# Kernel tuning notes

Measured on AMD Instinct MI355X. Metric: run time of the kernel, lower is better.

## Reference

```python
import jax, jax.numpy as jnp
import numpy as np

HIDDEN = 1024
HEADS = 16
HEAD_DIM = HIDDEN // HEADS
BATCH = 2
SEQ = 2048


def setup_inputs() -> dict:
    key = jax.random.key(0)
    k1, k2, k3 = jax.random.split(key, 3)
    hidden_states = jax.random.normal(k1, (BATCH, SEQ, HIDDEN), dtype=jnp.float32)
    # torch Linear(hidden, 3*hidden) applies x @ W.T; we store the transposed
    # weight directly so the math is x @ W_qkv. Scale ~ fan_in init.
    W_qkv = jax.random.normal(k2, (HIDDEN, 3 * HIDDEN), dtype=jnp.float32) / np.sqrt(HIDDEN)
    W_o = jax.random.normal(k3, (HIDDEN, HIDDEN), dtype=jnp.float32) / np.sqrt(HIDDEN)
    return {"hidden_states": hidden_states, "W_qkv": W_qkv, "W_o": W_o}


def reference(hidden_states, W_qkv, W_o):
    B, S, _ = hidden_states.shape
    scale = 1.0 / np.sqrt(HEAD_DIM)
    qkv = hidden_states @ W_qkv                       # [B, S, 3*H*D]
    qkv = qkv.reshape(B, S, 3, HEADS, HEAD_DIM)
    qkv = jnp.transpose(qkv, (2, 0, 3, 1, 4))         # [3, B, H, S, D]
    q, k, v = qkv[0], qkv[1], qkv[2]
    # The chunked online-softmax path computes exactly softmax(qk^T*scale)v.
    scores = jnp.einsum("bhsd,bhtd->bhst", q, k) * scale  # [B, H, S, S]
    probs = jax.nn.softmax(scores, axis=-1)
    out = jnp.einsum("bhst,bhtd->bhsd", probs, v)     # [B, H, S, D]
    out = jnp.transpose(out, (0, 2, 1, 3)).reshape(B, S, HIDDEN)
    return out @ W_o
```

## Files before the change

### kernel.cpp

```cpp
#include <hip/hip_runtime.h>
#include <hip/hip_bf16.h>
#include <cstdint>

typedef __bf16 bf16_t;
typedef __bf16 bf16x8 __attribute__((ext_vector_type(8)));
typedef __bf16 bf16x4 __attribute__((ext_vector_type(4)));
typedef __bf16 bf16x2 __attribute__((ext_vector_type(2)));
typedef float  f32x4  __attribute__((ext_vector_type(4)));
typedef float  f32x16 __attribute__((ext_vector_type(16)));
typedef unsigned uint4v __attribute__((ext_vector_type(4)));

#define AS1 __attribute__((address_space(1)))
#define AS3 __attribute__((address_space(3)))

static __device__ __forceinline__ void gld_lds16(const void* g, void* l) {
  __builtin_amdgcn_global_load_lds((AS1 void*)g, (AS3 void*)l, 16, 0, 0);
}

static __device__ __forceinline__ unsigned pk2t(float a, float b) {
  return __builtin_amdgcn_perm(__builtin_bit_cast(unsigned, a),
                               __builtin_bit_cast(unsigned, b), 0x03020706u);
}

__global__ __launch_bounds__(256) void prep_k(const float* __restrict__ x,
                                              bf16_t* __restrict__ xb,
                                              const float* __restrict__ wqkv,
                                              bf16_t* __restrict__ wqkvT,
                                              const float* __restrict__ wo,
                                              bf16_t* __restrict__ woT) {
  int bid = blockIdx.x;
  if (bid < 4096) {
    const int i = bid * 256 + threadIdx.x;
    float4 v = ((const float4*)x)[i];
    bf16x4 o;
    o[0] = (bf16_t)v.x; o[1] = (bf16_t)v.y; o[2] = (bf16_t)v.z; o[3] = (bf16_t)v.w;
    *(bf16x4*)(xb + (size_t)i * 4) = o;
    return;
  }
  __shared__ float tile[32][33];
  const float* in; bf16_t* out; int N, bx, by;
  if (bid < 7168) { bid -= 4096; in = wqkv; out = wqkvT; N = 3072; bx = bid % 96; by = bid / 96; }
  else            { bid -= 7168; in = wo;   out = woT;   N = 1024; bx = bid & 31; by = bid >> 5; }
  const int t = threadIdx.x, c = t & 31, r0 = t >> 5;
#pragma unroll
  for (int i = 0; i < 4; ++i) {
    int r = r0 + i * 8;
    tile[r][c] = in[(size_t)(by * 32 + r) * N + bx * 32 + c];
  }
  __syncthreads();
#pragma unroll
  for (int i = 0; i < 4; ++i) {
    int r = r0 + i * 8;
    out[(size_t)(bx * 32 + r) * 1024 + by * 32 + c] = (bf16_t)tile[c][r];
  }
}

template <int KDIM>
static __device__ __forceinline__ void gemm128_pipe(const bf16_t* __restrict__ A,
                                                    const bf16_t* __restrict__ Bt,
                                                    char* lds, f32x4 acc[4][4],
                                                    int bm, int bn) {
  constexpr int NK = KDIM / 32;
  const int t = threadIdx.x;
  const int lr = t & 15, g = (t >> 4) & 3;
  const int w = t >> 6, wr = w >> 1, wc = w & 1;

  auto bufA = [&](int i) { return lds + (i % 3) * 8192; };
  auto bufB = [&](int i) { return lds + 24576 + (i % 3) * 8192; };

  auto stage = [&](int i) {
    const int kt = i * 32;
    char* la = bufA(i);
    char* lb = bufB(i);
#pragma unroll
    for (int c = 0; c < 2; ++c) {
      const int idx = c * 256 + t;
      const int row = idx >> 2, cb = idx & 3;
      const int off = ((t & 192) + c * 256) * 16;
      gld_lds16(A  + (size_t)(bm * 128 + row) * KDIM + kt + cb * 8, la + off);
      gld_lds16(Bt + (size_t)(bn * 128 + row) * KDIM + kt + cb * 8, lb + off);
    }
  };

  stage(0);
  stage(1);
  asm volatile("s_waitcnt vmcnt(4)" ::: "memory");
  __builtin_amdgcn_sched_barrier(0);
  __builtin_amdgcn_s_barrier();

  for (int j = 0; j < NK; ++j) {
    if (j + 2 < NK) {
      stage(j + 2);
      asm volatile("s_waitcnt vmcnt(8)" ::: "memory");
    } else if (j + 1 < NK) {
      asm volatile("s_waitcnt vmcnt(4)" ::: "memory");
    } else {
      asm volatile("s_waitcnt vmcnt(0)" ::: "memory");
    }
    __builtin_amdgcn_sched_barrier(0);
    __builtin_amdgcn_s_barrier();
    const char* laR = bufA(j);
    const char* lbR = bufB(j);
    bf16x8 af[4], bv[4];
#pragma unroll
    for (int mi = 0; mi < 4; ++mi)
      af[mi] = *(const bf16x8*)(laR + (wr * 64 + mi * 16 + lr) * 64 + g * 16);
#pragma unroll
    for (int ni = 0; ni < 4; ++ni)
      bv[ni] = *(const bf16x8*)(lbR + (wc * 64 + ni * 16 + lr) * 64 + g * 16);
    __builtin_amdgcn_s_setprio(1);
#pragma unroll
    for (int mi = 0; mi < 4; ++mi)
#pragma unroll
      for (int ni = 0; ni < 4; ++ni)
        acc[mi][ni] = __builtin_amdgcn_mfma_f32_16x16x32_bf16(af[mi], bv[ni], acc[mi][ni], 0, 0, 0);
    __builtin_amdgcn_s_setprio(0);
    __builtin_amdgcn_sched_barrier(0);
    __builtin_amdgcn_s_barrier();
  }
}

__global__ __launch_bounds__(256) void gemm_qkv_k(const bf16_t* __restrict__ xb,
                                                  const bf16_t* __restrict__ wt,
                                                  bf16_t* __restrict__ Qo,
                                                  bf16_t* __restrict__ Ko,
                                                  bf16_t* __restrict__ Vto) {
  __shared__ __align__(16) char lds[49152];
  const int bm = blockIdx.x, bn = blockIdx.y;
  f32x4 acc[4][4] = {};
  gemm128_pipe<1024>(xb, wt, lds, acc, bm, bn);
  const float cs = 0.18033688011112042f;
  const int t = threadIdx.x, lr = t & 15, g = (t >> 4) & 3, w = t >> 6, wr = w >> 1, wc = w & 1;
  const int row0 = bm * 128 + wr * 64, col0 = bn * 128 + wc * 64;
#pragma unroll
  for (int mi = 0; mi < 4; ++mi) {
    const int row = row0 + mi * 16 + g * 4;
    const int b = row >> 11, s = row & 2047;
#pragma unroll
    for (int ni = 0; ni < 4; ++ni) {
      const int col = col0 + ni * 16 + lr;
      const int t3 = col >> 10, rem = col & 1023, h = rem >> 6, d = rem & 63;
      const int bh = b * 16 + h;
#pragma unroll
      for (int r = 0; r < 4; ++r) {
        const float av = acc[mi][ni][r];
        if (t3 == 0)      Qo[((size_t)bh * 2048 + s + r) * 64 + d] = (bf16_t)(av * cs);
        else if (t3 == 1) Ko[((size_t)bh * 2048 + s + r) * 64 + d] = (bf16_t)av;
        else {
          const int kv = s + r;
          const int q3 = (kv >> 2) & 7;
          const int dq = (q3 & 4) | ((q3 & 1) << 1) | ((q3 >> 1) & 1);
          const int kvp = (kv & ~31) | (dq << 2) | (kv & 3);
          Vto[((size_t)bh * 64 + d) * 2048 + kvp] = (bf16_t)av;
        }
      }
    }
  }
}

__global__ __launch_bounds__(256) void gemm_o_k(const bf16_t* __restrict__ attn,
                                                const bf16_t* __restrict__ wot,
                                                float* __restrict__ out) {
  __shared__ __align__(16) char lds[49152];
  const int bm = blockIdx.x, bn = blockIdx.y;
  f32x4 acc[4][4] = {};
  gemm128_pipe<1024>(attn, wot, lds, acc, bm, bn);
  const int t = threadIdx.x, lr = t & 15, g = (t >> 4) & 3, w = t >> 6, wr = w >> 1, wc = w & 1;
  const int row0 = bm * 128 + wr * 64, col0 = bn * 128 + wc * 64;
#pragma unroll
  for (int mi = 0; mi < 4; ++mi) {
    const int row = row0 + mi * 16 + g * 4;
#pragma unroll
    for (int ni = 0; ni < 4; ++ni) {
      const int col = col0 + ni * 16 + lr;
#pragma unroll
      for (int r = 0; r < 4; ++r)
        out[(size_t)(row + r) * 1024 + col] = acc[mi][ni][r];
    }
  }
}

__global__ __launch_bounds__(256, 2) void attn_k(const bf16_t* __restrict__ Q,
                                                 const bf16_t* __restrict__ K,
                                                 const bf16_t* __restrict__ Vt,
                                                 bf16_t* __restrict__ Ao) {
  __shared__ __align__(16) char smem[32768];
  const int t = threadIdx.x, w = t >> 6, l = t & 63;
  const int ql = l & 31, hi = l >> 5;
  const int orig = blockIdx.y * 16 + blockIdx.x;
  const int swz = (orig & 7) * 64 + (orig >> 3);
  const int qblk = swz & 15, bh = swz >> 4;
  const int b = bh >> 4, h = bh & 15;
  const bf16_t* Qb = Q  + (size_t)bh * 2048 * 64;
  const bf16_t* Kb = K  + (size_t)bh * 2048 * 64;
  const bf16_t* Vb = Vt + (size_t)bh * 64 * 2048;
  const int q0 = qblk * 128 + w * 32;

  const bf16_t* ksrc = Kb + (size_t)l * 64 + w * 8;
  const bf16_t* vsrc = Vb + (size_t)l * 2048 + w * 8;

  char* const kb0 = smem;
  char* const kb1 = smem + 8192;
  char* const vb0 = smem + 16384;
  char* const vb1 = smem + 24576;

  const bf16_t* qp = Qb + (size_t)(q0 + ql) * 64 + hi * 8;
  const bf16x8 qf0 = *(const bf16x8*)(qp);
  const bf16x8 qf1 = *(const bf16x8*)(qp + 16);
  const bf16x8 qf2 = *(const bf16x8*)(qp + 32);
  const bf16x8 qf3 = *(const bf16x8*)(qp + 48);

  bf16x8 ones;
#pragma unroll
  for (int i = 0; i < 8; ++i) ones[i] = (bf16_t)1.0f;

  f32x16 ot0 = {}, ot1 = {}, otls = {};

  auto stageK = [&](int tile, char* dst) {
    const bf16_t* ks = ksrc + (size_t)tile * 4096;
    gld_lds16(ks,      dst + w * 1024);
    gld_lds16(ks + 32, dst + (4 + w) * 1024);
  };
  auto stageV = [&](int tile, char* dst) {
    const bf16_t* vs = vsrc + (size_t)tile * 64;
    gld_lds16(vs,      dst + w * 1024);
    gld_lds16(vs + 32, dst + (4 + w) * 1024);
  };
  auto qk = [&](const char* kbuf, f32x16& sa, f32x16& sb) {
    const bf16x8 ka0 = *(const bf16x8*)(kbuf + (0 + hi) * 1024 + ql * 16);
    const bf16x8 ka1 = *(const bf16x8*)(kbuf + (2 + hi) * 1024 + ql * 16);
    const bf16x8 ka2 = *(const bf16x8*)(kbuf + (4 + hi) * 1024 + ql * 16);
    const bf16x8 ka3 = *(const bf16x8*)(kbuf + (6 + hi) * 1024 + ql * 16);
    sa = __builtin_amdgcn_mfma_f32_32x32x16_bf16(ka0, qf0, sa, 0, 0, 0);
    sa = __builtin_amdgcn_mfma_f32_32x32x16_bf16(ka1, qf1, sa, 0, 0, 0);
    sa = __builtin_amdgcn_mfma_f32_32x32x16_bf16(ka2, qf2, sa, 0, 0, 0);
    sa = __builtin_amdgcn_mfma_f32_32x32x16_bf16(ka3, qf3, sa, 0, 0, 0);
    const bf16x8 kb0f = *(const bf16x8*)(kbuf + (0 + hi) * 1024 + 512 + ql * 16);
    const bf16x8 kb1f = *(const bf16x8*)(kbuf + (2 + hi) * 1024 + 512 + ql * 16);
    const bf16x8 kb2f = *(const bf16x8*)(kbuf + (4 + hi) * 1024 + 512 + ql * 16);
    const bf16x8 kb3f = *(const bf16x8*)(kbuf + (6 + hi) * 1024 + 512 + ql * 16);
    sb = __builtin_amdgcn_mfma_f32_32x32x16_bf16(kb0f, qf0, sb, 0, 0, 0);
    sb = __builtin_amdgcn_mfma_f32_32x32x16_bf16(kb1f, qf1, sb, 0, 0, 0);
    sb = __builtin_amdgcn_mfma_f32_32x32x16_bf16(kb2f, qf2, sb, 0, 0, 0);
    sb = __builtin_amdgcn_mfma_f32_32x32x16_bf16(kb3f, qf3, sb, 0, 0, 0);
  };
  auto sm_pv = [&](const f32x16& sa, const f32x16& sb, const char* vread) {
    uint4v u0 = {pk2t(exp2f(sa[0]),  exp2f(sa[1])),  pk2t(exp2f(sa[2]),  exp2f(sa[3])),
                 pk2t(exp2f(sa[4]),  exp2f(sa[5])),  pk2t(exp2f(sa[6]),  exp2f(sa[7]))};
    uint4v u1 = {pk2t(exp2f(sa[8]),  exp2f(sa[9])),  pk2t(exp2f(sa[10]), exp2f(sa[11])),
                 pk2t(exp2f(sa[12]), exp2f(sa[13])), pk2t(exp2f(sa[14]), exp2f(sa[15]))};
    uint4v u2 = {pk2t(exp2f(sb[0]),  exp2f(sb[1])),  pk2t(exp2f(sb[2]),  exp2f(sb[3])),
                 pk2t(exp2f(sb[4]),  exp2f(sb[5])),  pk2t(exp2f(sb[6]),  exp2f(sb[7]))};
    uint4v u3 = {pk2t(exp2f(sb[8]),  exp2f(sb[9])),  pk2t(exp2f(sb[10]), exp2f(sb[11])),
                 pk2t(exp2f(sb[12]), exp2f(sb[13])), pk2t(exp2f(sb[14]), exp2f(sb[15]))};
    const bf16x8 pf0 = __builtin_bit_cast(bf16x8, u0);
    const bf16x8 pf1 = __builtin_bit_cast(bf16x8, u1);
    const bf16x8 pf2 = __builtin_bit_cast(bf16x8, u2);
    const bf16x8 pf3 = __builtin_bit_cast(bf16x8, u3);
    const bf16x8 v00 = *(const bf16x8*)(vread + (0 + hi) * 1024 + ql * 16);
    const bf16x8 v01 = *(const bf16x8*)(vread + (2 + hi) * 1024 + ql * 16);
    const bf16x8 v02 = *(const bf16x8*)(vread + (4 + hi) * 1024 + ql * 16);
    const bf16x8 v03 = *(const bf16x8*)(vread + (6 + hi) * 1024 + ql * 16);
    const bf16x8 v10 = *(const bf16x8*)(vread + (0 + hi) * 1024 + 512 + ql * 16);
    const bf16x8 v11 = *(const bf16x8*)(vread + (2 + hi) * 1024 + 512 + ql * 16);
    const bf16x8 v12 = *(const bf16x8*)(vread + (4 + hi) * 1024 + 512 + ql * 16);
    const bf16x8 v13 = *(const bf16x8*)(vread + (6 + hi) * 1024 + 512 + ql * 16);
    ot0  = __builtin_amdgcn_mfma_f32_32x32x16_bf16(v00,  pf0, ot0, 0, 0, 0);
    ot1  = __builtin_amdgcn_mfma_f32_32x32x16_bf16(v10,  pf0, ot1, 0, 0, 0);
    otls = __builtin_amdgcn_mfma_f32_32x32x16_bf16(ones, pf0, otls, 0, 0, 0);
    ot0  = __builtin_amdgcn_mfma_f32_32x32x16_bf16(v01,  pf1, ot0, 0, 0, 0);
    ot1  = __builtin_amdgcn_mfma_f32_32x32x16_bf16(v11,  pf1, ot1, 0, 0, 0);
    otls = __builtin_amdgcn_mfma_f32_32x32x16_bf16(ones, pf1, otls, 0, 0, 0);
    ot0  = __builtin_amdgcn_mfma_f32_32x32x16_bf16(v02,  pf2, ot0, 0, 0, 0);
    ot1  = __builtin_amdgcn_mfma_f32_32x32x16_bf16(v12,  pf2, ot1, 0, 0, 0);
    otls = __builtin_amdgcn_mfma_f32_32x32x16_bf16(ones, pf2, otls, 0, 0, 0);
    ot0  = __builtin_amdgcn_mfma_f32_32x32x16_bf16(v03,  pf3, ot0, 0, 0, 0);
    ot1  = __builtin_amdgcn_mfma_f32_32x32x16_bf16(v13,  pf3, ot1, 0, 0, 0);
    otls = __builtin_amdgcn_mfma_f32_32x32x16_bf16(ones, pf3, otls, 0, 0, 0);
  };

  stageK(0, kb0);
  stageV(0, vb0);
  stageK(1, kb1);
  asm volatile("s_waitcnt vmcnt(4)" ::: "memory");
  __builtin_amdgcn_sched_barrier(0);
  __builtin_amdgcn_s_barrier();
  f32x16 sca = {}, scb = {};
  qk(kb0, sca, scb);
  __builtin_amdgcn_s_barrier();

  auto body = [&](int j, char* kstage, const char* kread, const char* vread, char* vstage) {
    if (j < 31) stageV(j + 1, vstage);
    if (j < 30) stageK(j + 2, kstage);
    if (j < 30)      asm volatile("s_waitcnt vmcnt(4)" ::: "memory");
    else if (j == 30) asm volatile("s_waitcnt vmcnt(2)" ::: "memory");
    else             asm volatile("s_waitcnt vmcnt(0)" ::: "memory");
    __builtin_amdgcn_sched_barrier(0);
    __builtin_amdgcn_s_barrier();
    f32x16 sna = {}, snb = {};
    __builtin_amdgcn_s_setprio(1);
    if (j < 31) qk(kread, sna, snb);
    sm_pv(sca, scb, vread);
    __builtin_amdgcn_s_setprio(0);
    __builtin_amdgcn_sched_barrier(0);
    __builtin_amdgcn_s_barrier();
    sca = sna; scb = snb;
  };

#pragma unroll 2
  for (int j = 0; j < 32; ++j) {
    if ((j & 1) == 0) body(j, kb0, kb1, vb0, vb1);
    else              body(j, kb1, kb0, vb1, vb0);
  }

  const float inv = 1.0f / otls[0];
  bf16_t* ob = (bf16_t*)(smem + w * 4096);
#pragma unroll
  for (int rg = 0; rg < 4; ++rg) {
    const int d0 = rg * 8 + hi * 4;
    bf16x4 v0, v1;
#pragma unroll
    for (int j = 0; j < 4; ++j) {
      v0[j] = (bf16_t)(ot0[4 * rg + j] * inv);
      v1[j] = (bf16_t)(ot1[4 * rg + j] * inv);
    }
    *(bf16x4*)((char*)ob + ql * 128 + (((d0)      * 2) ^ ((ql & 7) << 4))) = v0;
    *(bf16x4*)((char*)ob + ql * 128 + (((d0 + 32) * 2) ^ ((ql & 7) << 4))) = v1;
  }
  __syncthreads();
#pragma unroll
  for (int i = 0; i < 4; ++i) {
    const int c = i * 64 + l;
    const int qq = c >> 3, ch = c & 7;
    bf16x8 vv = *(const bf16x8*)((char*)ob + qq * 128 + ((ch * 16) ^ ((qq & 7) << 4)));
    *(bf16x8*)(Ao + (size_t)(b * 2048 + q0 + qq) * 1024 + h * 64 + ch * 8) = vv;
  }
}


extern "C" void kernel_launch(void* const* d_in, const int* in_sizes, int n_in,
                              void* d_out, int out_size, void* d_ws, size_t ws_size,
                              hipStream_t stream) {
  const float* x    = (const float*)d_in[0];
  const float* wqkv = (const float*)d_in[1];
  const float* wo   = (const float*)d_in[2];
  float* out = (float*)d_out;

  char* ws = (char*)d_ws;
  bf16_t* xb    = (bf16_t*)(ws);
  bf16_t* wqkvT = (bf16_t*)(ws + (size_t)(8u  << 20));
  bf16_t* woT   = (bf16_t*)(ws + (size_t)(14u << 20));
  bf16_t* Qb    = (bf16_t*)(ws + (size_t)(16u << 20));
  bf16_t* Kb    = (bf16_t*)(ws + (size_t)(24u << 20));
  bf16_t* Vtb   = (bf16_t*)(ws + (size_t)(32u << 20));
  bf16_t* attn  = (bf16_t*)(ws + (size_t)(40u << 20));

  prep_k<<<8192, 256, 0, stream>>>(x, xb, wqkv, wqkvT, wo, woT);
  gemm_qkv_k<<<dim3(32, 24), 256, 0, stream>>>(xb, wqkvT, Qb, Kb, Vtb);
  attn_k<<<dim3(16, 32), 256, 0, stream>>>(Qb, Kb, Vtb, attn);
  gemm_o_k<<<dim3(32, 8), 256, 0, stream>>>(attn, woT, out);
}
```

Before: 119.0 us.

## Use triple-buffered K/V in attention and a single-barrier GEMM pipeline

The attention kernel moves from double- to triple-buffered K/V tiles in LDS (48KB) and issues the next stages after the per-iteration barrier, which drops the trailing barrier. The GEMM main loop is restructured the same way, with one barrier per k-step and prefetch issued after it. The x fp32-to-bf16 conversion now handles 8 elements per thread, so fewer blocks are launched. The larger LDS footprint per attention block may limit occupancy. Removing the trailing barriers relies on the three-buffer rotation to prevent overwriting tiles that other waves are still reading.

```diff
diff --git a/kernel.cpp b/kernel.cpp
--- a/kernel.cpp
+++ b/kernel.cpp
@@ -29,18 +29,20 @@
                                               const float* __restrict__ wo,
                                               bf16_t* __restrict__ woT) {
   int bid = blockIdx.x;
-  if (bid < 4096) {
+  if (bid < 2048) {
     const int i = bid * 256 + threadIdx.x;
-    float4 v = ((const float4*)x)[i];
-    bf16x4 o;
-    o[0] = (bf16_t)v.x; o[1] = (bf16_t)v.y; o[2] = (bf16_t)v.z; o[3] = (bf16_t)v.w;
-    *(bf16x4*)(xb + (size_t)i * 4) = o;
+    float4 v0 = ((const float4*)x)[(size_t)i * 2];
+    float4 v1 = ((const float4*)x)[(size_t)i * 2 + 1];
+    bf16x8 o;
+    o[0] = (bf16_t)v0.x; o[1] = (bf16_t)v0.y; o[2] = (bf16_t)v0.z; o[3] = (bf16_t)v0.w;
+    o[4] = (bf16_t)v1.x; o[5] = (bf16_t)v1.y; o[6] = (bf16_t)v1.z; o[7] = (bf16_t)v1.w;
+    *(bf16x8*)(xb + (size_t)i * 8) = o;
     return;
   }
   __shared__ float tile[32][33];
   const float* in; bf16_t* out; int N, bx, by;
-  if (bid < 7168) { bid -= 4096; in = wqkv; out = wqkvT; N = 3072; bx = bid % 96; by = bid / 96; }
-  else            { bid -= 7168; in = wo;   out = woT;   N = 1024; bx = bid & 31; by = bid >> 5; }
+  if (bid < 5120) { bid -= 2048; in = wqkv; out = wqkvT; N = 3072; bx = bid % 96; by = bid / 96; }
+  else            { bid -= 5120; in = wo;   out = woT;   N = 1024; bx = bid & 31; by = bid >> 5; }
   const int t = threadIdx.x, c = t & 31, r0 = t >> 5;
 #pragma unroll
   for (int i = 0; i < 4; ++i) {
@@ -84,21 +86,13 @@
 
   stage(0);
   stage(1);
-  asm volatile("s_waitcnt vmcnt(4)" ::: "memory");
-  __builtin_amdgcn_sched_barrier(0);
-  __builtin_amdgcn_s_barrier();
 
   for (int j = 0; j < NK; ++j) {
-    if (j + 2 < NK) {
-      stage(j + 2);
-      asm volatile("s_waitcnt vmcnt(8)" ::: "memory");
-    } else if (j + 1 < NK) {
-      asm volatile("s_waitcnt vmcnt(4)" ::: "memory");
-    } else {
-      asm volatile("s_waitcnt vmcnt(0)" ::: "memory");
-    }
+    if (j < NK - 1) asm volatile("s_waitcnt vmcnt(4)" ::: "memory");
+    else            asm volatile("s_waitcnt vmcnt(0)" ::: "memory");
     __builtin_amdgcn_sched_barrier(0);
     __builtin_amdgcn_s_barrier();
+    if (j + 2 < NK) stage(j + 2);
     const char* laR = bufA(j);
     const char* lbR = bufB(j);
     bf16x8 af[4], bv[4];
@@ -115,8 +109,6 @@
       for (int ni = 0; ni < 4; ++ni)
         acc[mi][ni] = __builtin_amdgcn_mfma_f32_16x16x32_bf16(af[mi], bv[ni], acc[mi][ni], 0, 0, 0);
     __builtin_amdgcn_s_setprio(0);
-    __builtin_amdgcn_sched_barrier(0);
-    __builtin_amdgcn_s_barrier();
   }
 }
 
@@ -184,7 +176,7 @@
                                                  const bf16_t* __restrict__ K,
                                                  const bf16_t* __restrict__ Vt,
                                                  bf16_t* __restrict__ Ao) {
-  __shared__ __align__(16) char smem[32768];
+  __shared__ __align__(16) char smem[49152];
   const int t = threadIdx.x, w = t >> 6, l = t & 63;
   const int ql = l & 31, hi = l >> 5;
   const int orig = blockIdx.y * 16 + blockIdx.x;
@@ -198,11 +190,6 @@
 
   const bf16_t* ksrc = Kb + (size_t)l * 64 + w * 8;
   const bf16_t* vsrc = Vb + (size_t)l * 2048 + w * 8;
-
-  char* const kb0 = smem;
-  char* const kb1 = smem + 8192;
-  char* const vb0 = smem + 16384;
-  char* const vb1 = smem + 24576;
 
   const bf16_t* qp = Qb + (size_t)(q0 + ql) * 64 + hi * 8;
   const bf16x8 qf0 = *(const bf16x8*)(qp);
@@ -279,53 +266,53 @@
     otls = __builtin_amdgcn_mfma_f32_32x32x16_bf16(ones, pf3, otls, 0, 0, 0);
   };
 
-  stageK(0, kb0);
-  stageV(0, vb0);
-  stageK(1, kb1);
-  asm volatile("s_waitcnt vmcnt(4)" ::: "memory");
+  char *k0 = smem,          *k1 = smem + 8192,          *k2 = smem + 16384;
+  char *v0 = smem + 24576,  *v1 = smem + 32768,         *v2 = smem + 40960;
+
+  stageK(0, k0);
+  stageV(0, v0);
+  stageK(1, k1);
+  stageV(1, v1);
+  stageK(2, k2);
+  asm volatile("s_waitcnt vmcnt(8)" ::: "memory");
   __builtin_amdgcn_sched_barrier(0);
   __builtin_amdgcn_s_barrier();
   f32x16 sca = {}, scb = {};
-  qk(kb0, sca, scb);
-  __builtin_amdgcn_s_barrier();
-
-  auto body = [&](int j, char* kstage, const char* kread, const char* vread, char* vstage) {
-    if (j < 31) stageV(j + 1, vstage);
-    if (j < 30) stageK(j + 2, kstage);
-    if (j < 30)      asm volatile("s_waitcnt vmcnt(4)" ::: "memory");
+  qk(k0, sca, scb);
+
+  for (int j = 0; j < 32; ++j) {
+    if (j <= 29)      asm volatile("s_waitcnt vmcnt(4)" ::: "memory");
     else if (j == 30) asm volatile("s_waitcnt vmcnt(2)" ::: "memory");
-    else             asm volatile("s_waitcnt vmcnt(0)" ::: "memory");
+    else              asm volatile("s_waitcnt vmcnt(0)" ::: "memory");
     __builtin_amdgcn_sched_barrier(0);
     __builtin_amdgcn_s_barrier();
+    if (j + 2 < 32) stageV(j + 2, v2);
+    if (j + 3 < 32) stageK(j + 3, k0);
     f32x16 sna = {}, snb = {};
     __builtin_amdgcn_s_setprio(1);
-    if (j < 31) qk(kread, sna, snb);
-    sm_pv(sca, scb, vread);
+    if (j < 31) qk(k1, sna, snb);
+    sm_pv(sca, scb, v0);
     __builtin_amdgcn_s_setprio(0);
-    __builtin_amdgcn_sched_barrier(0);
-    __builtin_amdgcn_s_barrier();
     sca = sna; scb = snb;
-  };
-
-#pragma unroll 2
-  for (int j = 0; j < 32; ++j) {
-    if ((j & 1) == 0) body(j, kb0, kb1, vb0, vb1);
-    else              body(j, kb1, kb0, vb1, vb0);
-  }
+    char* tk = k0; k0 = k1; k1 = k2; k2 = tk;
+    char* tv = v0; v0 = v1; v1 = v2; v2 = tv;
+  }
+
+  __syncthreads();
 
   const float inv = 1.0f / otls[0];
   bf16_t* ob = (bf16_t*)(smem + w * 4096);
 #pragma unroll
   for (int rg = 0; rg < 4; ++rg) {
     const int d0 = rg * 8 + hi * 4;
-    bf16x4 v0, v1;
+    bf16x4 w0, w1;
 #pragma unroll
     for (int j = 0; j < 4; ++j) {
-      v0[j] = (bf16_t)(ot0[4 * rg + j] * inv);
-      v1[j] = (bf16_t)(ot1[4 * rg + j] * inv);
+      w0[j] = (bf16_t)(ot0[4 * rg + j] * inv);
+      w1[j] = (bf16_t)(ot1[4 * rg + j] * inv);
     }
-    *(bf16x4*)((char*)ob + ql * 128 + (((d0)      * 2) ^ ((ql & 7) << 4))) = v0;
-    *(bf16x4*)((char*)ob + ql * 128 + (((d0 + 32) * 2) ^ ((ql & 7) << 4))) = v1;
+    *(bf16x4*)((char*)ob + ql * 128 + (((d0)      * 2) ^ ((ql & 7) << 4))) = w0;
+    *(bf16x4*)((char*)ob + ql * 128 + (((d0 + 32) * 2) ^ ((ql & 7) << 4))) = w1;
   }
   __syncthreads();
 #pragma unroll
@@ -355,7 +342,7 @@
   bf16_t* Vtb   = (bf16_t*)(ws + (size_t)(32u << 20));
   bf16_t* attn  = (bf16_t*)(ws + (size_t)(40u << 20));
 
-  prep_k<<<8192, 256, 0, stream>>>(x, xb, wqkv, wqkvT, wo, woT);
+  prep_k<<<6144, 256, 0, stream>>>(x, xb, wqkv, wqkvT, wo, woT);
   gemm_qkv_k<<<dim3(32, 24), 256, 0, stream>>>(xb, wqkvT, Qb, Kb, Vtb);
   attn_k<<<dim3(16, 32), 256, 0, stream>>>(Qb, Kb, Vtb, attn);
   gemm_o_k<<<dim3(32, 8), 256, 0, stream>>>(attn, woT, out);
```

New measurement: 121.3 us. No clear change (+1.9%).
